# Optimization experiments

Hardware: AMD Instinct MI355X
Metric: run time of the kernel (lower is better)

Reference implementation:

```python
import jax, jax.numpy as jnp
import numpy as np

T, B, V, NG, H, MLP = 1024, 128, 128, 10, 1024, 128
F = V + NG  # feature_size = alphabet one-hot + genre one-hot


def setup_inputs() -> dict:
    key = jax.random.key(0)
    ks = jax.random.split(key, 14)
    s = 0.02
    inp = {
        "x": jax.random.normal(ks[0], (T, B, F), dtype=jnp.float32),
        # LSTMCell 1: input F -> hidden H (PyTorch layout: W_ih [4H, F], W_hh [4H, H])
        "W_ih1": jax.random.normal(ks[1], (4 * H, F), dtype=jnp.float32) * s,
        "b_ih1": jax.random.normal(ks[2], (4 * H,), dtype=jnp.float32) * s,
        "W_hh1": jax.random.normal(ks[3], (4 * H, H), dtype=jnp.float32) * s,
        "b_hh1": jax.random.normal(ks[4], (4 * H,), dtype=jnp.float32) * s,
        # LSTMCell 2: H -> H
        "W_ih2": jax.random.normal(ks[5], (4 * H, H), dtype=jnp.float32) * s,
        "b_ih2": jax.random.normal(ks[6], (4 * H,), dtype=jnp.float32) * s,
        "W_hh2": jax.random.normal(ks[7], (4 * H, H), dtype=jnp.float32) * s,
        "b_hh2": jax.random.normal(ks[8], (4 * H,), dtype=jnp.float32) * s,
        # MLP head: Linear(H,128) -> SELU -> Linear(128, V). Dropout(0.2) is identity in eval.
        "W1": jax.random.normal(ks[9], (MLP, H), dtype=jnp.float32) * s,
        "b1": jax.random.normal(ks[10], (MLP,), dtype=jnp.float32) * s,
        "W2": jax.random.normal(ks[11], (V, MLP), dtype=jnp.float32) * s,
        "b2": jax.random.normal(ks[12], (V,), dtype=jnp.float32) * s,
        "predict": 0,
    }
    return inp


def _lstm_cell(xt, h, c, W_ih, b_ih, W_hh, b_hh):
    # PyTorch LSTMCell gate order: input, forget, cell(g), output
    gates = xt @ W_ih.T + b_ih + h @ W_hh.T + b_hh  # [B, 4H]
    i, f, g, o = jnp.split(gates, 4, axis=-1)
    i, f, o = jax.nn.sigmoid(i), jax.nn.sigmoid(f), jax.nn.sigmoid(o)
    g = jnp.tanh(g)
    c_new = f * c + i * g
    h_new = o * jnp.tanh(c_new)
    return h_new, c_new


def reference(x, W_ih1, b_ih1, W_hh1, b_hh1, W_ih2, b_ih2, W_hh2, b_hh2,
              W1, b1, W2, b2, predict):
    n = x.shape[1]
    h0 = jnp.zeros((n, H), dtype=jnp.float32)
    init = (h0, h0, h0, h0)  # h_t, c_t, h2_t, c2_t

    def step(carry, xt):
        h, c, h2, c2 = carry
        h, c = _lstm_cell(xt, h, c, W_ih1, b_ih1, W_hh1, b_hh1)
        h2, c2 = _lstm_cell(h, h2, c2, W_ih2, b_ih2, W_hh2, b_hh2)
        out = jax.nn.selu(h2 @ W1.T + b1) @ W2.T + b2  # [B, V]
        return (h, c, h2, c2), out

    _, outputs = jax.lax.scan(step, init, x)  # [T, B, V]
    return outputs
```

## Files before the change

### kernel.cpp

```cpp
#include <hip/hip_runtime.h>
#include <cstdint>
#include <cstddef>

#define TT   1024
#define BB   128
#define FEAT 138
#define FPAD 160
#define HH   1024
#define VV   128
#define MM   128
#define K1   1184
#define K1P  1280
#define K2   2048
#define HCH  1024
#define H1N  131072
#define MIDN 16384
#define PKM1 1032
#define PKM2 136
#define OFF_RED 0
#define OFF_WM  32768
#define OFF_H   65792
#define OFF_M   67840
#define LDSZ    68864

typedef __bf16 bf16x8 __attribute__((ext_vector_type(8)));
typedef float  f32x4  __attribute__((ext_vector_type(4)));
typedef unsigned short u16;

__device__ __forceinline__ u16 f2bf(float f) {
  uint32_t u = __float_as_uint(f);
  u += 0x7fffu + ((u >> 16) & 1u);
  return (u16)(u >> 16);
}
__device__ __forceinline__ float sigm(float x) { return 1.0f / (1.0f + __expf(-x)); }
__device__ __forceinline__ float tanh_(float x) {
  float e = __expf(-2.0f * fabsf(x));
  float t = (1.0f - e) / (1.0f + e);
  return x < 0.0f ? -t : t;
}

__device__ __forceinline__ void stcc16(u16* p, uint4 v) {
  unsigned long long* p64 = (unsigned long long*)p;
  unsigned long long lo = ((unsigned long long)v.y << 32) | v.x;
  unsigned long long hi = ((unsigned long long)v.w << 32) | v.z;
  __hip_atomic_store(p64,     lo, __ATOMIC_RELAXED, __HIP_MEMORY_SCOPE_AGENT);
  __hip_atomic_store(p64 + 1, hi, __ATOMIC_RELAXED, __HIP_MEMORY_SCOPE_AGENT);
}

__global__ void conv_w1i(const float* __restrict__ Wih, const float* __restrict__ Whh,
                         const float* __restrict__ bi, const float* __restrict__ bh,
                         u16* __restrict__ dst, float* __restrict__ bsum) {
  int rp = blockIdx.x;
  int hc = rp >> 2, g = rp & 3;
  int sr = g * HH + hc;
  if (threadIdx.x == 0) bsum[rp] = bi[sr] + bh[sr];
  for (int k = threadIdx.x; k < K1P; k += 256) {
    float v = 0.0f;
    if (k < FPAD)    v = (k < FEAT) ? Wih[(size_t)sr * FEAT + k] : 0.0f;
    else if (k < K1) v = Whh[(size_t)sr * HH + (k - FPAD)];
    dst[(size_t)rp * K1P + k] = f2bf(v);
  }
}
__global__ void conv_w2i(const float* __restrict__ Wih, const float* __restrict__ Whh,
                         const float* __restrict__ bi, const float* __restrict__ bh,
                         u16* __restrict__ dst, float* __restrict__ bsum) {
  int rp = blockIdx.x;
  int hc = rp >> 2, g = rp & 3;
  int sr = g * HH + hc;
  if (threadIdx.x == 0) bsum[rp] = bi[sr] + bh[sr];
  for (int k = threadIdx.x; k < K2; k += 256) {
    float v = (k < HH) ? Wih[(size_t)sr * HH + k] : Whh[(size_t)sr * HH + (k - HH)];
    dst[(size_t)rp * K2 + k] = f2bf(v);
  }
}
__global__ void conv_mlpw(const float* __restrict__ W1, const float* __restrict__ W2,
                          u16* __restrict__ A, u16* __restrict__ Bm) {
  int i = blockIdx.x * 256 + threadIdx.x;
  if (i < MM * HH) A[i] = f2bf(W1[i]);
  else {
    int j = i - MM * HH;
    if (j < VV * MM) Bm[j] = f2bf(W2[j]);
  }
}
__global__ void conv_x(const float* __restrict__ x, u16* __restrict__ Xb) {
  int blk = blockIdx.x;
  int t = blk / 20, c = blk % 20;
  int b = threadIdx.x;
  if (b >= BB) return;
  const float* src = x + ((size_t)t * BB + b) * FEAT;
  u16 v[8];
#pragma unroll
  for (int e = 0; e < 8; ++e) {
    int col = c * 8 + e;
    v[e] = (col < FEAT) ? f2bf(src[col]) : (u16)0;
  }
  *(uint4*)(Xb + (((size_t)t * 20 + c) * BB + b) * 8) = *(uint4*)v;
}
__global__ void zero_ws(uint4* __restrict__ p, int n16) {
  int i = blockIdx.x * 256 + threadIdx.x;
  if (i < n16) p[i] = uint4{0, 0, 0, 0};
}


__device__ __forceinline__ void mfma_tile(const bf16x8& a0, const bf16x8& a1,
                                          const bf16x8 (&B)[4], f32x4 (&acc)[2][4]) {
#pragma unroll
  for (int n = 0; n < 4; ++n) {
    acc[0][n] = __builtin_amdgcn_mfma_f32_16x16x32_bf16(a0, B[n], acc[0][n], 0, 0, 0);
    acc[1][n] = __builtin_amdgcn_mfma_f32_16x16x32_bf16(a1, B[n], acc[1][n], 0, 0, 0);
  }
}
__device__ __forceinline__ void ld_tile(const u16* __restrict__ p, bf16x8 (&B)[4]) {
#pragma unroll
  for (int n = 0; n < 4; ++n) B[n] = *(const bf16x8*)(p + n * 128);
}
template<int NT, int OFS, int NA>
__device__ __forceinline__ void mac_ring(const bf16x8 (&A0)[NA], const bf16x8 (&A1)[NA],
                                         const u16* __restrict__ bp,
                                         f32x4 (&acc)[2][4]) {
  constexpr int D = NT < 4 ? NT : 4;
  bf16x8 Bq[D][4];
#pragma unroll
  for (int s = 0; s < D; ++s) ld_tile(bp + (size_t)s * 4096, Bq[s]);
#pragma unroll
  for (int s = 0; s < NT; ++s) {
    mfma_tile(A0[OFS + s], A1[OFS + s], Bq[s % D], acc);
    if (s + D < NT) ld_tile(bp + (size_t)(s + D) * 4096, Bq[s % D]);
  }
}
__device__ __forceinline__ void mac_step(const bf16x8& a0, const bf16x8& a1,
                                         const u16* __restrict__ bptr,
                                         f32x4 (&acc)[2][4]) {
  bf16x8 Bf[4];
  ld_tile(bptr, Bf);
  mfma_tile(a0, a1, Bf, acc);
}

__device__ __forceinline__ void red_write(float* __restrict__ rg,
                                          const f32x4 (&acc)[2][4], int lane) {
#pragma unroll
  for (int mt = 0; mt < 2; ++mt)
#pragma unroll
    for (int n = 0; n < 4; ++n)
      *(f32x4*)(rg + (mt * 4 + n) * 256 + lane * 4) = acc[mt][n];
}
__device__ __forceinline__ void red_add(const float* __restrict__ rg,
                                        f32x4 (&acc)[2][4], int lane) {
#pragma unroll
  for (int mt = 0; mt < 2; ++mt)
#pragma unroll
    for (int n = 0; n < 4; ++n)
      acc[mt][n] += *(const f32x4*)(rg + (mt * 4 + n) * 256 + lane * 4);
}

__device__ __forceinline__ void lstm_tail(f32x4 (&acc)[2][4], const f32x4& bsv0,
                                          const f32x4& bsv1, float (&cst)[2][4],
                                          char* smem, int bh, int lane, int q, int l16,
                                          u16* __restrict__ houtChunk) {
  u16* st = (u16*)(smem + OFF_H) + bh * 512;
#pragma unroll
  for (int mt = 0; mt < 2; ++mt) {
    const f32x4 bsv = mt ? bsv1 : bsv0;
#pragma unroll
    for (int n = 0; n < 4; ++n) {
      float iv = sigm(acc[mt][n][0] + bsv[0]);
      float fv = sigm(acc[mt][n][1] + bsv[1]);
      float gv = tanh_(acc[mt][n][2] + bsv[2]);
      float ov = sigm(acc[mt][n][3] + bsv[3]);
      float c = fv * cst[mt][n] + iv * gv;
      cst[mt][n] = c;
      st[(n * 16 + l16) * 8 + mt * 4 + q] = f2bf(ov * tanh_(c));
    }
  }
  uint4 hv4 = *(uint4*)((u16*)(smem + OFF_H) + bh * 512 + lane * 8);
  stcc16(houtChunk + ((size_t)bh * 64 + lane) * 8, hv4);
}

__device__ __forceinline__ void gbar(unsigned* __restrict__ bar, unsigned g) {
  asm volatile("s_waitcnt vmcnt(0)" ::: "memory");
  __syncthreads();
  if (threadIdx.x == 0) {
    unsigned v = __hip_atomic_fetch_add(&bar[(blockIdx.x & 7) * 16], 1u,
                                        __ATOMIC_RELAXED, __HIP_MEMORY_SCOPE_AGENT);
    if (v == 32u * g - 1u) {
      unsigned w = __hip_atomic_fetch_add(&bar[128], 1u,
                                          __ATOMIC_RELAXED, __HIP_MEMORY_SCOPE_AGENT);
      if (w == 8u * g - 1u)
        __hip_atomic_store(&bar[144], g, __ATOMIC_RELAXED, __HIP_MEMORY_SCOPE_AGENT);
    }
    __builtin_amdgcn_fence(__ATOMIC_ACQUIRE, "agent");
    while (__hip_atomic_load(&bar[144], __ATOMIC_RELAXED,
                             __HIP_MEMORY_SCOPE_AGENT) < g)
      __builtin_amdgcn_s_sleep(1);
  }
  __syncthreads();
}

template<int MODE>
__global__ __launch_bounds__(512, 2) void fused_lstm(
    const u16* __restrict__ W1i, const u16* __restrict__ W2i,
    const u16* __restrict__ W1m, const u16* __restrict__ W2m,
    const u16* __restrict__ Xb, u16* __restrict__ h1b, u16* __restrict__ h2b,
    u16* __restrict__ h2h, u16* __restrict__ midb,
    const float* __restrict__ bs1, const float* __restrict__ bs2,
    const float* __restrict__ bm1, const float* __restrict__ bm2,
    float* __restrict__ out, unsigned* __restrict__ bar)
{
  extern __shared__ char smem[];
  const int tid = threadIdx.x, bid = blockIdx.x;
  const int w = tid >> 6, lane = tid & 63, q = lane >> 4, l16 = lane & 15;
  const int kw = w & 3, bh = w >> 2;
  const bool isL1 = bid < 128;
  const int j = isL1 ? bid : bid - 128;
  float* red = (float*)(smem + OFF_RED);
  u16* Wm = (u16*)(smem + OFF_WM);
  const int PEND = MODE ? (TT + 1) : (TT + 3);

  float cst[2][4] = {{0, 0, 0, 0}, {0, 0, 0, 0}};
  f32x4 bsv0 = {0, 0, 0, 0}, bsv1 = {0, 0, 0, 0};
  if (kw == 0) {
    const float* bs = isL1 ? bs1 : bs2;
    bsv0 = *(const f32x4*)(bs + (j * 8 + q) * 4);
    bsv1 = *(const f32x4*)(bs + (j * 8 + 4 + q) * 4);
  }

  if (isL1) {
    bf16x8 A1[2][10];
#pragma unroll
    for (int mt = 0; mt < 2; ++mt)
#pragma unroll
      for (int s = 0; s < 10; ++s)
        A1[mt][s] = *(const bf16x8*)(W1i + (size_t)(j * 32 + mt * 16 + l16) * K1P +
                                     (size_t)(kw * 10 + s) * 32 + q * 8);
    f32x4 bmv = {0, 0, 0, 0};
    if constexpr (MODE == 0) {
      if (j < 64) {
        int m0 = (j & 7) * 16;
        for (int i = tid; i < 16 * 128; i += 512) {
          int r = i >> 7, c8 = i & 127;
          *(uint4*)(Wm + r * PKM1 + c8 * 8) =
              *(const uint4*)(W1m + ((size_t)(m0 + r)) * HH + c8 * 8);
        }
      } else {
        int v0 = ((j - 64) & 7) * 16;
        for (int i = tid; i < 16 * 16; i += 512) {
          int r = i >> 4, c8 = i & 15;
          *(uint4*)(Wm + r * PKM2 + c8 * 8) =
              *(const uint4*)(W2m + ((size_t)(v0 + r)) * MM + c8 * 8);
        }
      }
      if (w == 3) {
        if (j < 64) bmv = *(const f32x4*)(bm1 + (j & 7) * 16 + q * 4);
        else        bmv = *(const f32x4*)(bm2 + ((j - 64) & 7) * 16 + q * 4);
      }
      __syncthreads();
    }

    for (int p = 0; p < PEND; ++p) {
      const bool act = p < TT;
      if (act) {
        const u16* h1p = h1b + (size_t)((p - 1) & 1) * H1N;
        f32x4 acc[2][4];
#pragma unroll
        for (int mt = 0; mt < 2; ++mt)
#pragma unroll
          for (int n = 0; n < 4; ++n) acc[mt][n] = (f32x4){0, 0, 0, 0};
        if (kw == 0) {
          const u16* bx = Xb + (size_t)p * 20480 +
                          ((size_t)q * 128 + bh * 64 + l16) * 8;
          mac_ring<5, 0, 10>(A1[0], A1[1], bx, acc);
          const u16* bp = h1p + ((size_t)q * 128 + bh * 64 + l16) * 8;
          mac_ring<5, 5, 10>(A1[0], A1[1], bp, acc);
        } else {
          const u16* bp = h1p + ((size_t)((kw * 10 - 5) * 4 + q) * 128 +
                                 bh * 64 + l16) * 8;
          if (kw == 3) mac_ring<7, 0, 10>(A1[0], A1[1], bp, acc);
          else         mac_ring<10, 0, 10>(A1[0], A1[1], bp, acc);
        }
        if (kw >= 2) red_write(red + (bh * 2 + kw - 2) * 2048, acc, lane);
        __syncthreads();
        if (kw < 2)  red_add(red + (bh * 2 + kw) * 2048, acc, lane);
        if (kw == 1) red_write(red + (bh * 2 + 1) * 2048, acc, lane);
        __syncthreads();
        if (kw == 0) {
          red_add(red + (bh * 2 + 1) * 2048, acc, lane);
          lstm_tail(acc, bsv0, bsv1, cst, smem, bh, lane, q, l16,
                    h1b + (size_t)(p & 1) * H1N + (size_t)j * HCH);
        }
      }
      if constexpr (MODE == 0) {
        if (w == 3) {
          if (j < 64) {
            if (p >= 2 && p <= TT + 1) {
              int jm = j & 7, jb = j >> 3;
              const u16* bsrc = h2b + (size_t)(p & 1) * H1N + q * HCH +
                                (jb * 16 + l16) * 8;
              const u16* am = Wm + l16 * PKM1 + q * 8;
              f32x4 acc = {0, 0, 0, 0};
#pragma unroll 4
              for (int s = 0; s < 32; ++s) {
                bf16x8 bf = *(const bf16x8*)(bsrc + (size_t)s * 4096);
                bf16x8 af = *(const bf16x8*)(am + s * 32);
                acc = __builtin_amdgcn_mfma_f32_16x16x32_bf16(af, bf, acc, 0, 0, 0);
              }
              const float SC = 1.0507009873554804934193349852946f;
              const float AL = 1.6732632423543772848170429916717f;
              u16* st16 = (u16*)(smem + OFF_M);
#pragma unroll
              for (int r = 0; r < 4; ++r) {
                float v = acc[r] + bmv[r];
                v = v > 0.0f ? SC * v : SC * AL * (__expf(v) - 1.0f);
                st16[l16 * 16 + q * 4 + r] = f2bf(v);
              }
              if (lane < 16) {
                uint4 v0 = *(uint4*)(st16 + lane * 16);
                uint4 v1 = *(uint4*)(st16 + lane * 16 + 8);
                u16* mc = midb + (size_t)(p & 1) * MIDN;
                stcc16(mc + (size_t)(2 * jm) * HCH + (jb * 16 + lane) * 8, v0);
                stcc16(mc + (size_t)(2 * jm + 1) * HCH + (jb * 16 + lane) * 8, v1);
              }
            }
          } else if (p >= 3) {
            int jj = j - 64, jv = jj & 7, jb = jj >> 3;
            const u16* bsrc = midb + (size_t)((p - 3) & 1) * MIDN + q * HCH +
                              (jb * 16 + l16) * 8;
            const u16* am = Wm + l16 * PKM2 + q * 8;
            f32x4 acc = {0, 0, 0, 0};
#pragma unroll
            for (int s = 0; s < 4; ++s) {
              bf16x8 bf = *(const bf16x8*)(bsrc + (size_t)s * 4096);
              bf16x8 af = *(const bf16x8*)(am + s * 32);
              acc = __builtin_amdgcn_mfma_f32_16x16x32_bf16(af, bf, acc, 0, 0, 0);
            }
            float* stf = (float*)(smem + OFF_M);
#pragma unroll
            for (int r = 0; r < 4; ++r) stf[l16 * 16 + q * 4 + r] = acc[r] + bmv[r];
            if (lane < 16) {
              float* orow = out + ((size_t)(p - 3) * BB + jb * 16 + lane) * VV + jv * 16;
              uint4* s4 = (uint4*)(stf + lane * 16);
              *(uint4*)(orow + 0)  = s4[0];
              *(uint4*)(orow + 4)  = s4[1];
              *(uint4*)(orow + 8)  = s4[2];
              *(uint4*)(orow + 12) = s4[3];
            }
          }
        }
      }
      gbar(bar, (unsigned)p + 1u);
    }
  } else {
    bf16x8 A2[2][16];
#pragma unroll
    for (int mt = 0; mt < 2; ++mt)
#pragma unroll
      for (int s = 0; s < 16; ++s)
        A2[mt][s] = *(const bf16x8*)(W2i + (size_t)(j * 32 + mt * 16 + l16) * K2 +
                                     (size_t)(kw * 16 + s) * 32 + q * 8);

    for (int p = 0; p < PEND; ++p) {
      const bool act = (p >= 1 && p <= TT);
      if (act) {
        const int t = p - 1;
        const u16* h1c = h1b + (size_t)(t & 1) * H1N;
        const u16* h2p = MODE ? (h2h + (size_t)t * H1N)
                              : (h2b + (size_t)((t - 1) & 1) * H1N);
        const u16* src = (kw < 2) ? h1c : h2p;
        const u16* bbase = src + ((size_t)((kw & 1) * 64 + q) * 128 +
                                  bh * 64 + l16) * 8;
        f32x4 acc[2][4];
#pragma unroll
        for (int mt = 0; mt < 2; ++mt)
#pragma unroll
          for (int n = 0; n < 4; ++n) acc[mt][n] = (f32x4){0, 0, 0, 0};
        mac_ring<16, 0, 16>(A2[0], A2[1], bbase, acc);

        if (kw >= 2) red_write(red + (bh * 2 + kw - 2) * 2048, acc, lane);
        __syncthreads();
        if (kw < 2)  red_add(red + (bh * 2 + kw) * 2048, acc, lane);
        if (kw == 1) red_write(red + (bh * 2 + 1) * 2048, acc, lane);
        __syncthreads();
        if (kw == 0) {
          red_add(red + (bh * 2 + 1) * 2048, acc, lane);
          u16* dst = MODE ? (h2h + (size_t)(t + 1) * H1N + (size_t)j * HCH)
                          : (h2b + (size_t)(t & 1) * H1N + (size_t)j * HCH);
          lstm_tail(acc, bsv0, bsv1, cst, smem, bh, lane, q, l16, dst);
        }
      }
      gbar(bar, (unsigned)p + 1u);
    }
  }
}

__global__ __launch_bounds__(256) void mlp_head(
    const u16* __restrict__ W1m, const u16* __restrict__ W2m,
    const u16* __restrict__ h2h, const float* __restrict__ b1,
    const float* __restrict__ b2, float* __restrict__ out)
{
  __shared__ u16 midl[16 * 128 * 8];
  const int tid = threadIdx.x, t = blockIdx.x;
  const int wid = tid >> 6, lane = tid & 63, q = lane >> 4, l16 = lane & 15;
  const u16* h2t = h2h + (size_t)(t + 1) * H1N;
  const int mbase = wid * 32;

  f32x4 acc[2][8];
#pragma unroll
  for (int a = 0; a < 2; ++a)
#pragma unroll
    for (int n = 0; n < 8; ++n) acc[a][n] = (f32x4){0, 0, 0, 0};
#pragma unroll 2
  for (int kc = 0; kc < 32; ++kc) {
    bf16x8 a0 = *(const bf16x8*)(W1m + (size_t)(mbase + l16) * HH + kc * 32 + q * 8);
    bf16x8 a1 = *(const bf16x8*)(W1m + (size_t)(mbase + 16 + l16) * HH + kc * 32 + q * 8);
    const u16* bp = h2t + (size_t)(kc * 4 + q) * 1024 + l16 * 8;
#pragma unroll
    for (int n = 0; n < 8; ++n) {
      bf16x8 bf = *(const bf16x8*)(bp + n * 128);
      acc[0][n] = __builtin_amdgcn_mfma_f32_16x16x32_bf16(a0, bf, acc[0][n], 0, 0, 0);
      acc[1][n] = __builtin_amdgcn_mfma_f32_16x16x32_bf16(a1, bf, acc[1][n], 0, 0, 0);
    }
  }
  const float SC = 1.0507009873554804934193349852946f;
  const float AL = 1.6732632423543772848170429916717f;
  f32x4 bm0 = *(const f32x4*)(b1 + mbase + q * 4);
  f32x4 bm1v = *(const f32x4*)(b1 + mbase + 16 + q * 4);
#pragma unroll
  for (int mt = 0; mt < 2; ++mt) {
    const f32x4 bm = mt ? bm1v : bm0;
    const int m0 = mbase + mt * 16 + q * 4;
#pragma unroll
    for (int n = 0; n < 8; ++n) {
      const int b = n * 16 + l16;
#pragma unroll
      for (int r = 0; r < 4; ++r) {
        float v = acc[mt][n][r] + bm[r];
        v = v > 0.0f ? SC * v : SC * AL * (__expf(v) - 1.0f);
        int mm = m0 + r;
        midl[(mm >> 3) * 1024 + b * 8 + (mm & 7)] = f2bf(v);
      }
    }
  }
  __syncthreads();
  f32x4 acc2[2][8];
#pragma unroll
  for (int a = 0; a < 2; ++a)
#pragma unroll
    for (int n = 0; n < 8; ++n) acc2[a][n] = (f32x4){0, 0, 0, 0};
#pragma unroll
  for (int kc = 0; kc < 4; ++kc) {
    bf16x8 a0 = *(const bf16x8*)(W2m + (size_t)(mbase + l16) * MM + kc * 32 + q * 8);
    bf16x8 a1 = *(const bf16x8*)(W2m + (size_t)(mbase + 16 + l16) * MM + kc * 32 + q * 8);
    const u16* bp = midl + (kc * 4 + q) * 1024 + l16 * 8;
#pragma unroll
    for (int n = 0; n < 8; ++n) {
      bf16x8 bf = *(const bf16x8*)(bp + n * 128);
      acc2[0][n] = __builtin_amdgcn_mfma_f32_16x16x32_bf16(a0, bf, acc2[0][n], 0, 0, 0);
      acc2[1][n] = __builtin_amdgcn_mfma_f32_16x16x32_bf16(a1, bf, acc2[1][n], 0, 0, 0);
    }
  }
  f32x4 c0 = *(const f32x4*)(b2 + mbase + q * 4);
  f32x4 c1 = *(const f32x4*)(b2 + mbase + 16 + q * 4);
  float* ot = out + (size_t)t * BB * VV;
#pragma unroll
  for (int mt = 0; mt < 2; ++mt)
#pragma unroll
    for (int n = 0; n < 8; ++n) {
      f32x4 v = acc2[mt][n] + (mt ? c1 : c0);
      *(f32x4*)(ot + (size_t)(n * 16 + l16) * VV + mbase + mt * 16 + q * 4) = v;
    }
}

extern "C" void kernel_launch(void* const* d_in, const int* in_sizes, int n_in,
                              void* d_out, int out_size, void* d_ws, size_t ws_size,
                              hipStream_t stream)
{
  const float* x    = (const float*)d_in[0];
  const float* Wih1 = (const float*)d_in[1];
  const float* bih1 = (const float*)d_in[2];
  const float* Whh1 = (const float*)d_in[3];
  const float* bhh1 = (const float*)d_in[4];
  const float* Wih2 = (const float*)d_in[5];
  const float* bih2 = (const float*)d_in[6];
  const float* Whh2 = (const float*)d_in[7];
  const float* bhh2 = (const float*)d_in[8];
  const float* W1   = (const float*)d_in[9];
  const float* b1   = (const float*)d_in[10];
  const float* W2   = (const float*)d_in[11];
  const float* b2   = (const float*)d_in[12];
  float* out = (float*)d_out;
  (void)in_sizes; (void)n_in; (void)out_size;

  char* ws = (char*)d_ws;
  size_t off = 0;
  auto alloc = [&](size_t n) { char* p = ws + off; off += (n + 255) & ~(size_t)255; return p; };
  u16* W1i   = (u16*)alloc((size_t)4096 * K1P * 2);
  u16* W2i   = (u16*)alloc((size_t)4096 * K2 * 2);
  u16* W1m   = (u16*)alloc((size_t)MM * HH * 2);
  u16* W2m   = (u16*)alloc((size_t)VV * MM * 2);
  u16* Xb    = (u16*)alloc((size_t)TT * 20 * BB * 8 * 2);
  float* bs1 = (float*)alloc(4096 * 4);
  float* bs2 = (float*)alloc(4096 * 4);
  u16* h1b   = (u16*)alloc(2 * (size_t)H1N * 2 + 32768);
  u16* h2b   = (u16*)alloc(2 * (size_t)H1N * 2);
  u16* midb  = (u16*)alloc(2 * (size_t)MIDN * 2);
  unsigned* bar = (unsigned*)alloc(4096);
  size_t off_base = off;
  u16* h2h   = (u16*)alloc((size_t)(TT + 1) * H1N * 2);
  const bool postMLP = ws_size >= off;
  if (ws_size < off_base) return;

  conv_w1i<<<4096, 256, 0, stream>>>(Wih1, Whh1, bih1, bhh1, W1i, bs1);
  conv_w2i<<<4096, 256, 0, stream>>>(Wih2, Whh2, bih2, bhh2, W2i, bs2);
  conv_mlpw<<<576, 256, 0, stream>>>(W1, W2, W1m, W2m);
  conv_x<<<TT * 20, 128, 0, stream>>>(x, Xb);
  {
    int n16 = (int)((2 * (size_t)H1N * 2 + 32768 + 2 * (size_t)H1N * 2 +
                     2 * (size_t)MIDN * 2 + 4096) / 16);
    zero_ws<<<(n16 + 255) / 256, 256, 0, stream>>>((uint4*)h1b, n16);
  }
  if (postMLP) {
    zero_ws<<<(H1N * 2 / 16 + 255) / 256, 256, 0, stream>>>((uint4*)h2h, H1N * 2 / 16);
  }

  using KFn = void (*)(const u16*, const u16*, const u16*, const u16*, const u16*,
                       u16*, u16*, u16*, u16*, const float*, const float*,
                       const float*, const float*, float*, unsigned*);
  KFn fp = postMLP ? (KFn)fused_lstm<1> : (KFn)fused_lstm<0>;
  (void)hipFuncSetAttribute((const void*)fp,
                            hipFuncAttributeMaxDynamicSharedMemorySize, LDSZ);
  void* args[] = { (void*)&W1i, (void*)&W2i, (void*)&W1m, (void*)&W2m,
                   (void*)&Xb, (void*)&h1b, (void*)&h2b, (void*)&h2h, (void*)&midb,
                   (void*)&bs1, (void*)&bs2, (void*)&b1, (void*)&b2,
                   (void*)&out, (void*)&bar };
  hipError_t err = hipLaunchCooperativeKernel((const void*)fp,
                                              dim3(256), dim3(512), args, LDSZ, stream);
  if (err != hipSuccess) {
    if (postMLP)
      fused_lstm<1><<<dim3(256), dim3(512), LDSZ, stream>>>(
          W1i, W2i, W1m, W2m, Xb, h1b, h2b, h2h, midb, bs1, bs2, b1, b2, out, bar);
    else
      fused_lstm<0><<<dim3(256), dim3(512), LDSZ, stream>>>(
          W1i, W2i, W1m, W2m, Xb, h1b, h2b, h2h, midb, bs1, bs2, b1, b2, out, bar);
  }
  if (postMLP) {
    mlp_head<<<dim3(TT), dim3(256), 0, stream>>>(W1m, W2m, h2h, b1, b2, out);
  }
}
```

Measured before the change: 14.72 ms.

## Replace grid-wide barrier with per-block progress flags in post-MLP mode

In the mode where the MLP head runs as a separate kernel, the grid barrier after each timestep is replaced by per-block progress flags. Each block publishes its completed phase, and consumers wait only until layer-1 blocks reach phase p and layer-2 blocks reach p-2 (for layer 1) or p. The layer-1 hidden-state buffer grows from double to quadruple buffering so layer 1 can run ahead of layer 2 without overwriting states still being read. The aim is to cut barrier latency and let the two layers pipeline more loosely, at the cost of more polling traffic and an extra buffer.

```diff
diff --git a/kernel.cpp b/kernel.cpp
--- a/kernel.cpp
+++ b/kernel.cpp
@@ -128,13 +128,6 @@
     if (s + D < NT) ld_tile(bp + (size_t)(s + D) * 4096, Bq[s % D]);
   }
 }
-__device__ __forceinline__ void mac_step(const bf16x8& a0, const bf16x8& a1,
-                                         const u16* __restrict__ bptr,
-                                         f32x4 (&acc)[2][4]) {
-  bf16x8 Bf[4];
-  ld_tile(bptr, Bf);
-  mfma_tile(a0, a1, Bf, acc);
-}
 
 __device__ __forceinline__ void red_write(float* __restrict__ rg,
                                           const f32x4 (&acc)[2][4], int lane) {
@@ -174,6 +167,30 @@
   }
   uint4 hv4 = *(uint4*)((u16*)(smem + OFF_H) + bh * 512 + lane * 8);
   stcc16(houtChunk + ((size_t)bh * 64 + lane) * 8, hv4);
+}
+
+template<bool ISL1>
+__device__ __forceinline__ void wait_phase(const int* __restrict__ F, int p, int lane) {
+  if (threadIdx.x < 64) {
+    const int pa = p;
+    const int pb = ISL1 ? p - 2 : p;
+    for (;;) {
+      int a = __hip_atomic_load(F + lane,       __ATOMIC_RELAXED, __HIP_MEMORY_SCOPE_AGENT);
+      int b = __hip_atomic_load(F + 64 + lane,  __ATOMIC_RELAXED, __HIP_MEMORY_SCOPE_AGENT);
+      int c = __hip_atomic_load(F + 128 + lane, __ATOMIC_RELAXED, __HIP_MEMORY_SCOPE_AGENT);
+      int d = __hip_atomic_load(F + 192 + lane, __ATOMIC_RELAXED, __HIP_MEMORY_SCOPE_AGENT);
+      if (__all(a >= pa && b >= pa && c >= pb && d >= pb)) break;
+      __builtin_amdgcn_s_sleep(1);
+    }
+    __builtin_amdgcn_fence(__ATOMIC_ACQUIRE, "agent");
+  }
+  __syncthreads();
+}
+__device__ __forceinline__ void done_phase(int* __restrict__ slot, int p) {
+  asm volatile("s_waitcnt vmcnt(0)" ::: "memory");
+  __syncthreads();
+  if (threadIdx.x == 0)
+    __hip_atomic_store(slot, p + 1, __ATOMIC_RELAXED, __HIP_MEMORY_SCOPE_AGENT);
 }
 
 __device__ __forceinline__ void gbar(unsigned* __restrict__ bar, unsigned g) {
@@ -214,6 +231,8 @@
   const int j = isL1 ? bid : bid - 128;
   float* red = (float*)(smem + OFF_RED);
   u16* Wm = (u16*)(smem + OFF_WM);
+  int* flags = (int*)bar;
+  const int SM = MODE ? 3 : 1;
   const int PEND = MODE ? (TT + 1) : (TT + 3);
 
   float cst[2][4] = {{0, 0, 0, 0}, {0, 0, 0, 0}};
@@ -257,9 +276,10 @@
     }
 
     for (int p = 0; p < PEND; ++p) {
+      if constexpr (MODE == 1) wait_phase<true>(flags, p, lane);
       const bool act = p < TT;
       if (act) {
-        const u16* h1p = h1b + (size_t)((p - 1) & 1) * H1N;
+        const u16* h1p = h1b + (size_t)((p - 1) & SM) * H1N;
         f32x4 acc[2][4];
 #pragma unroll
         for (int mt = 0; mt < 2; ++mt)
@@ -285,7 +305,7 @@
         if (kw == 0) {
           red_add(red + (bh * 2 + 1) * 2048, acc, lane);
           lstm_tail(acc, bsv0, bsv1, cst, smem, bh, lane, q, l16,
-                    h1b + (size_t)(p & 1) * H1N + (size_t)j * HCH);
+                    h1b + (size_t)(p & SM) * H1N + (size_t)j * HCH);
         }
       }
       if constexpr (MODE == 0) {
@@ -345,8 +365,10 @@
             }
           }
         }
+        gbar(bar, (unsigned)p + 1u);
+      } else {
+        done_phase(flags + bid, p);
       }
-      gbar(bar, (unsigned)p + 1u);
     }
   } else {
     bf16x8 A2[2][16];
@@ -358,10 +380,11 @@
                                      (size_t)(kw * 16 + s) * 32 + q * 8);
 
     for (int p = 0; p < PEND; ++p) {
+      if constexpr (MODE == 1) wait_phase<false>(flags, p, lane);
       const bool act = (p >= 1 && p <= TT);
       if (act) {
         const int t = p - 1;
-        const u16* h1c = h1b + (size_t)(t & 1) * H1N;
+        const u16* h1c = h1b + (size_t)(t & SM) * H1N;
         const u16* h2p = MODE ? (h2h + (size_t)t * H1N)
                               : (h2b + (size_t)((t - 1) & 1) * H1N);
         const u16* src = (kw < 2) ? h1c : h2p;
@@ -386,7 +409,8 @@
           lstm_tail(acc, bsv0, bsv1, cst, smem, bh, lane, q, l16, dst);
         }
       }
-      gbar(bar, (unsigned)p + 1u);
+      if constexpr (MODE == 0) gbar(bar, (unsigned)p + 1u);
+      else                     done_phase(flags + bid, p);
     }
   }
 }
@@ -499,7 +523,7 @@
   u16* Xb    = (u16*)alloc((size_t)TT * 20 * BB * 8 * 2);
   float* bs1 = (float*)alloc(4096 * 4);
   float* bs2 = (float*)alloc(4096 * 4);
-  u16* h1b   = (u16*)alloc(2 * (size_t)H1N * 2 + 32768);
+  u16* h1b   = (u16*)alloc(4 * (size_t)H1N * 2 + 32768);
   u16* h2b   = (u16*)alloc(2 * (size_t)H1N * 2);
   u16* midb  = (u16*)alloc(2 * (size_t)MIDN * 2);
   unsigned* bar = (unsigned*)alloc(4096);
@@ -513,7 +537,7 @@
   conv_mlpw<<<576, 256, 0, stream>>>(W1, W2, W1m, W2m);
   conv_x<<<TT * 20, 128, 0, stream>>>(x, Xb);
   {
-    int n16 = (int)((2 * (size_t)H1N * 2 + 32768 + 2 * (size_t)H1N * 2 +
+    int n16 = (int)((4 * (size_t)H1N * 2 + 32768 + 2 * (size_t)H1N * 2 +
                      2 * (size_t)MIDN * 2 + 4096) / 16);
     zero_ws<<<(n16 + 255) / 256, 256, 0, stream>>>((uint4*)h1b, n16);
   }
```

New measurement: 14.74 ms. Within noise of the previous version (+0.1%).
